# Kernel optimization log

Measured on AMD Instinct MI355X. Metric: run time of the kernel, lower is better.

Reference implementation:

```python
import jax, jax.numpy as jnp
import numpy as np

VOCAB, EMBED, HIDDEN = 29, 64, 256
B, SEQ = 8, 257  # T = SEQ-1 = 256


def setup_inputs() -> dict:
    key = jax.random.key(0)
    ks = jax.random.split(key, 16)
    s = 0.02
    embed = jax.random.normal(ks[0], (VOCAB, EMBED), jnp.float32) * s
    embed = embed.at[0].set(0.0)  # padding_idx = PAD_TOKEN = 0
    d = dict(
        x=jax.random.randint(ks[1], (B, SEQ), 0, VOCAB),
        embed=embed,
        W_ih0=jax.random.normal(ks[2], (HIDDEN, EMBED), jnp.float32) * s,
        b_ih0=jax.random.normal(ks[3], (HIDDEN,), jnp.float32) * s,
        W_hh0=jax.random.normal(ks[4], (HIDDEN, HIDDEN), jnp.float32) * s,
        b_hh0=jax.random.normal(ks[5], (HIDDEN,), jnp.float32) * s,
        W_ih1=jax.random.normal(ks[6], (HIDDEN, HIDDEN), jnp.float32) * s,
        b_ih1=jax.random.normal(ks[7], (HIDDEN,), jnp.float32) * s,
        W_hh1=jax.random.normal(ks[8], (HIDDEN, HIDDEN), jnp.float32) * s,
        b_hh1=jax.random.normal(ks[9], (HIDDEN,), jnp.float32) * s,
        Wq=jax.random.normal(ks[10], (HIDDEN, HIDDEN), jnp.float32) * s,
        Wk=jax.random.normal(ks[11], (HIDDEN, HIDDEN), jnp.float32) * s,
        v=jax.random.normal(ks[12], (HIDDEN,), jnp.float32) * s,
        Wfc=jax.random.normal(ks[13], (VOCAB, 2 * HIDDEN), jnp.float32) * s,
        bfc=jax.random.normal(ks[14], (VOCAB,), jnp.float32) * s,
    )
    return d


def _forward(x, embed, W_ih0, b_ih0, W_hh0, b_hh0, W_ih1, b_ih1, W_hh1, b_hh1,
             Wq, Wk, v, Wfc, bfc):
    inp = x[:, :-1]                       # (B, T)
    emb = embed[inp]                      # (B, T, E); dropout = identity (eval)
    Bb, T, _ = emb.shape
    H = W_hh0.shape[0]

    # 2-layer Elman RNN via scan over time
    def step(carry, e_t):
        h0, h1 = carry
        h0 = jnp.tanh(e_t @ W_ih0.T + b_ih0 + h0 @ W_hh0.T + b_hh0)
        h1 = jnp.tanh(h0 @ W_ih1.T + b_ih1 + h1 @ W_hh1.T + b_hh1)
        return (h0, h1), h1

    init = (jnp.zeros((Bb, H), emb.dtype), jnp.zeros((Bb, H), emb.dtype))
    _, hs = jax.lax.scan(step, init, jnp.swapaxes(emb, 0, 1))  # (T, B, H)
    Hs = jnp.swapaxes(hs, 0, 1)           # (B, T, H) = all_hidden

    # Bahdanau additive self-attention over strictly-past hidden states
    q = Hs @ Wq.T                         # (B, T, H)
    k = Hs @ Wk.T                         # (B, T, H)
    e = jnp.tanh(q[:, :, None, :] + k[:, None, :, :])   # (B, T, T, H)
    scores = jnp.einsum('btsh,h->bts', e, v)             # (B, T, T)
    causal = jnp.tril(jnp.ones((T, T), bool), k=-1)      # s < t strictly
    scores = jnp.where(causal[None], scores, jnp.float32(-1e9))
    alpha = jax.nn.softmax(scores, axis=-1)
    ctx = jnp.einsum('bts,bsh->bth', alpha, Hs)          # (B, T, H)
    ctx = ctx * (jnp.arange(T) > 0)[None, :, None]       # t=0: zero context

    out = jnp.concatenate([Hs, ctx], axis=-1) @ Wfc.T + bfc  # (B, T, V)
    return out


def reference(x, embed, W_ih0, b_ih0, W_hh0, b_hh0, W_ih1, b_ih1, W_hh1, b_hh1,
              Wq, Wk, v, Wfc, bfc):
    return _forward(x, embed, W_ih0, b_ih0, W_hh0, b_hh0, W_ih1, b_ih1,
                    W_hh1, b_hh1, Wq, Wk, v, Wfc, bfc)
```

## Files before the change

### kernel.cpp

```cpp
#include <hip/hip_runtime.h>

#define HID   256
#define BATCH 8
#define TT    256
#define SEQL  257
#define VOCAB 29
#define EMB   64
#define TG    4
#define CH    8
#define NCHK  (TT / CH)

typedef _Float16 f16;
typedef f16  f16x8 __attribute__((ext_vector_type(8)));
typedef float f32x4 __attribute__((ext_vector_type(4)));

__device__ __forceinline__ float fast_tanh(float x) {
    float e = exp2f(x * 2.8853900817779268f);
    return 1.0f - 2.0f * __builtin_amdgcn_rcpf(1.0f + e);
}

__global__ __launch_bounds__(512) void mega_kernel(
    const int* __restrict__ x, const float* __restrict__ embed,
    const float* __restrict__ Wih0, const float* __restrict__ bih0,
    const float* __restrict__ bhh0, const float* __restrict__ Whh0,
    const float* __restrict__ Wih1, const float* __restrict__ Whh1,
    const float* __restrict__ bih1, const float* __restrict__ bhh1,
    const float* __restrict__ Wq, const float* __restrict__ Wk,
    float* __restrict__ C0, float* __restrict__ Q,
    float* __restrict__ Hs, float* __restrict__ tkT, int* __restrict__ flags)
{
    __shared__ f16 hbuf[2][HID];
    __shared__ __align__(16) f16 stg[CH][HID];
    __shared__ float er[CH][EMB];
    int tid = threadIdx.x;
    int wave = tid >> 6, lane = tid & 63;
    int lrow = lane & 15, lkg = lane >> 4;
    int role = blockIdx.x >> 3;
    int b = blockIdx.x & 7;
    int i0 = wave * 32 + lrow, i1 = i0 + 16;
    const f32x4 Z = {0.f, 0.f, 0.f, 0.f};

#define WAITF(idx, val)                                                             \
    {                                                                               \
        if (tid == 0) {                                                             \
            while (__hip_atomic_load(&flags[idx], __ATOMIC_ACQUIRE,                 \
                                     __HIP_MEMORY_SCOPE_AGENT) < (val))             \
                __builtin_amdgcn_s_sleep(2);                                        \
        }                                                                           \
        __syncthreads();                                                            \
    }
#define POSTF(idx, val)                                                             \
    {                                                                               \
        __syncthreads();                                                            \
        if (tid == 0) {                                                             \
            __threadfence();                                                        \
            __hip_atomic_store(&flags[idx], (val), __ATOMIC_RELEASE,                \
                               __HIP_MEMORY_SCOPE_AGENT);                           \
        }                                                                           \
    }

    f16x8 a[8];
#pragma unroll
    for (int kt = 0; kt < 8; ++kt)
#pragma unroll
        for (int e = 0; e < 8; ++e) a[kt][e] = (f16)0.f;

    if (role == 0) {
        int i = tid & 255, half = tid >> 8;
        float base = bih0[i] + bhh0[i];
        const float* wr = Wih0 + i * EMB;
        for (int ch = 0; ch < NCHK; ++ch) {
            int tb = ch * CH;
            { int tt = tid >> 6, j = tid & 63;
              er[tt][j] = embed[x[b * SEQL + tb + tt] * EMB + j]; }
            __syncthreads();
            float a0 = base, a1 = base, a2 = base, a3 = base;
            for (int j = 0; j < EMB; j += 4) {
                float4 w = *(const float4*)&wr[j];
                float4 h0 = *(const float4*)&er[half * 4 + 0][j];
                float4 h1 = *(const float4*)&er[half * 4 + 1][j];
                float4 h2 = *(const float4*)&er[half * 4 + 2][j];
                float4 h3 = *(const float4*)&er[half * 4 + 3][j];
                a0 += h0.x * w.x + h0.y * w.y + h0.z * w.z + h0.w * w.w;
                a1 += h1.x * w.x + h1.y * w.y + h1.z * w.z + h1.w * w.w;
                a2 += h2.x * w.x + h2.y * w.y + h2.z * w.z + h2.w * w.w;
                a3 += h3.x * w.x + h3.y * w.y + h3.z * w.z + h3.w * w.w;
            }
            C0[((size_t)(tb + half * 4 + 0) * BATCH + b) * HID + i] = a0;
            C0[((size_t)(tb + half * 4 + 1) * BATCH + b) * HID + i] = a1;
            C0[((size_t)(tb + half * 4 + 2) * BATCH + b) * HID + i] = a2;
            C0[((size_t)(tb + half * 4 + 3) * BATCH + b) * HID + i] = a3;
            POSTF(b, ch + 1)
        }
    } else if (role == 1) {
        for (int idx = tid; idx < 2 * HID; idx += 512) ((f16*)hbuf)[idx] = (f16)0.f;
        f16x8 bf[8][2];
#pragma unroll
        for (int kt = 0; kt < 8; ++kt)
#pragma unroll
            for (int ct = 0; ct < 2; ++ct) {
                int n = wave * 32 + ct * 16 + lrow;
                const float* src = Whh0 + n * HID + kt * 32 + lkg * 8;
                f16x8 v;
#pragma unroll
                for (int e = 0; e < 8; ++e) v[e] = (f16)src[e];
                bf[kt][ct] = v;
            }
        __syncthreads();
        const float* cp = C0 + b * HID;
        float c0 = 0.f, c1 = 0.f;
        f16* hp = (f16*)(Q + (size_t)b * TT * HID);

#define ASTEP(CUR, NXT)                                                             \
    {                                                                               \
        float cn0 = cp[i0];                                                         \
        float cn1 = cp[i1];                                                         \
        cp += BATCH * HID;                                                          \
        if (lrow == 0) {                                                            \
            _Pragma("unroll")                                                       \
            for (int kt = 0; kt < 8; ++kt)                                          \
                a[kt] = *(const f16x8*)&hbuf[CUR][kt * 32 + lkg * 8];               \
        }                                                                           \
        f32x4 p00 = __builtin_amdgcn_mfma_f32_16x16x32_f16(a[0], bf[0][0], Z, 0, 0, 0); \
        f32x4 p01 = __builtin_amdgcn_mfma_f32_16x16x32_f16(a[0], bf[0][1], Z, 0, 0, 0); \
        f32x4 p10 = __builtin_amdgcn_mfma_f32_16x16x32_f16(a[2], bf[2][0], Z, 0, 0, 0); \
        f32x4 p11 = __builtin_amdgcn_mfma_f32_16x16x32_f16(a[2], bf[2][1], Z, 0, 0, 0); \
        f32x4 p20 = __builtin_amdgcn_mfma_f32_16x16x32_f16(a[4], bf[4][0], Z, 0, 0, 0); \
        f32x4 p21 = __builtin_amdgcn_mfma_f32_16x16x32_f16(a[4], bf[4][1], Z, 0, 0, 0); \
        f32x4 p30 = __builtin_amdgcn_mfma_f32_16x16x32_f16(a[6], bf[6][0], Z, 0, 0, 0); \
        f32x4 p31 = __builtin_amdgcn_mfma_f32_16x16x32_f16(a[6], bf[6][1], Z, 0, 0, 0); \
        p00 = __builtin_amdgcn_mfma_f32_16x16x32_f16(a[1], bf[1][0], p00, 0, 0, 0); \
        p01 = __builtin_amdgcn_mfma_f32_16x16x32_f16(a[1], bf[1][1], p01, 0, 0, 0); \
        p10 = __builtin_amdgcn_mfma_f32_16x16x32_f16(a[3], bf[3][0], p10, 0, 0, 0); \
        p11 = __builtin_amdgcn_mfma_f32_16x16x32_f16(a[3], bf[3][1], p11, 0, 0, 0); \
        p20 = __builtin_amdgcn_mfma_f32_16x16x32_f16(a[5], bf[5][0], p20, 0, 0, 0); \
        p21 = __builtin_amdgcn_mfma_f32_16x16x32_f16(a[5], bf[5][1], p21, 0, 0, 0); \
        p30 = __builtin_amdgcn_mfma_f32_16x16x32_f16(a[7], bf[7][0], p30, 0, 0, 0); \
        p31 = __builtin_amdgcn_mfma_f32_16x16x32_f16(a[7], bf[7][1], p31, 0, 0, 0); \
        float v0 = fast_tanh(((p00[0] + p10[0]) + (p20[0] + p30[0])) + c0);         \
        float v1 = fast_tanh(((p01[0] + p11[0]) + (p21[0] + p31[0])) + c1);         \
        f16 hv0 = (f16)v0, hv1 = (f16)v1;                                           \
        if (lane < 16) {                                                            \
            hbuf[NXT][i0] = hv0;                                                    \
            hbuf[NXT][i1] = hv1;                                                    \
            hp[i0] = hv0;                                                           \
            hp[i1] = hv1;                                                           \
        }                                                                           \
        hp += 2 * HID;                                                              \
        c0 = cn0; c1 = cn1;                                                         \
        asm volatile("s_waitcnt lgkmcnt(0)\n\ts_barrier" ::: "memory");             \
    }

        for (int ch = 0; ch < NCHK; ++ch) {
            WAITF(b, (ch + 2 < NCHK) ? ch + 2 : NCHK)
            if (ch == 0) { c0 = cp[i0]; c1 = cp[i1]; cp += BATCH * HID; }
            ASTEP(0, 1) ASTEP(1, 0) ASTEP(0, 1) ASTEP(1, 0)
            ASTEP(0, 1) ASTEP(1, 0) ASTEP(0, 1) ASTEP(1, 0)
            POSTF(8 + b, ch + 1)
        }
#undef ASTEP
    } else if (role == 2) {
        f16x8 bfI[8][2];
#pragma unroll
        for (int kt = 0; kt < 8; ++kt)
#pragma unroll
            for (int ct = 0; ct < 2; ++ct) {
                int n = wave * 32 + ct * 16 + lrow;
                const float* src = Wih1 + n * HID + kt * 32 + lkg * 8;
                f16x8 v;
#pragma unroll
                for (int e = 0; e < 8; ++e) v[e] = (f16)src[e];
                bfI[kt][ct] = v;
            }
        int col0 = wave * 32 + (lane & 15), col1 = col0 + 16;
        float bv0 = bih1[col0] + bhh1[col0];
        float bv1 = bih1[col1] + bhh1[col1];
        float* qb = Q + (size_t)b * TT * HID;

        for (int ch = 0; ch < NCHK; ++ch) {
            WAITF(8 + b, ch + 1)
            if (tid < 256) {
                int tp = tid >> 5, seg = tid & 31;
                *(f16x8*)&stg[tp][seg * 8] =
                    *(const f16x8*)((const f16*)(qb + (size_t)(ch * CH + tp) * HID) + seg * 8);
            }
            __syncthreads();
            if (lrow < 8) {
#pragma unroll
                for (int kt = 0; kt < 8; ++kt)
                    a[kt] = *(const f16x8*)&stg[lrow][kt * 32 + lkg * 8];
            }
            f32x4 u0 = __builtin_amdgcn_mfma_f32_16x16x32_f16(a[0], bfI[0][0], Z, 0, 0, 0);
            f32x4 u1 = __builtin_amdgcn_mfma_f32_16x16x32_f16(a[0], bfI[0][1], Z, 0, 0, 0);
#pragma unroll
            for (int kt = 1; kt < 8; ++kt) {
                u0 = __builtin_amdgcn_mfma_f32_16x16x32_f16(a[kt], bfI[kt][0], u0, 0, 0, 0);
                u1 = __builtin_amdgcn_mfma_f32_16x16x32_f16(a[kt], bfI[kt][1], u1, 0, 0, 0);
            }
            if (lane < 32) {
                float* co = qb + (size_t)(ch * CH + (lane >> 4) * 4) * HID;
                co[0 * HID + col0] = u0[0] + bv0;
                co[1 * HID + col0] = u0[1] + bv0;
                co[2 * HID + col0] = u0[2] + bv0;
                co[3 * HID + col0] = u0[3] + bv0;
                co[0 * HID + col1] = u1[0] + bv1;
                co[1 * HID + col1] = u1[1] + bv1;
                co[2 * HID + col1] = u1[2] + bv1;
                co[3 * HID + col1] = u1[3] + bv1;
            }
            POSTF(16 + b, ch + 1)
        }
    } else if (role == 3) {
        for (int idx = tid; idx < 2 * HID; idx += 512) ((f16*)hbuf)[idx] = (f16)0.f;
        f16x8 bf[8][2];
#pragma unroll
        for (int kt = 0; kt < 8; ++kt)
#pragma unroll
            for (int ct = 0; ct < 2; ++ct) {
                int n = wave * 32 + ct * 16 + lrow;
                const float* src = Whh1 + n * HID + kt * 32 + lkg * 8;
                f16x8 v;
#pragma unroll
                for (int e = 0; e < 8; ++e) v[e] = (f16)src[e];
                bf[kt][ct] = v;
            }
        __syncthreads();
        float* ho = Hs + (size_t)b * TT * HID;
        const float* cq = Q + (size_t)b * TT * HID;

#define CSTEP(CUR, NXT, CV0, CV1)                                                   \
    {                                                                               \
        if (lrow == 0) {                                                            \
            _Pragma("unroll")                                                       \
            for (int kt = 0; kt < 8; ++kt)                                          \
                a[kt] = *(const f16x8*)&hbuf[CUR][kt * 32 + lkg * 8];               \
        }                                                                           \
        f32x4 p00 = __builtin_amdgcn_mfma_f32_16x16x32_f16(a[0], bf[0][0], Z, 0, 0, 0); \
        f32x4 p01 = __builtin_amdgcn_mfma_f32_16x16x32_f16(a[0], bf[0][1], Z, 0, 0, 0); \
        f32x4 p10 = __builtin_amdgcn_mfma_f32_16x16x32_f16(a[2], bf[2][0], Z, 0, 0, 0); \
        f32x4 p11 = __builtin_amdgcn_mfma_f32_16x16x32_f16(a[2], bf[2][1], Z, 0, 0, 0); \
        f32x4 p20 = __builtin_amdgcn_mfma_f32_16x16x32_f16(a[4], bf[4][0], Z, 0, 0, 0); \
        f32x4 p21 = __builtin_amdgcn_mfma_f32_16x16x32_f16(a[4], bf[4][1], Z, 0, 0, 0); \
        f32x4 p30 = __builtin_amdgcn_mfma_f32_16x16x32_f16(a[6], bf[6][0], Z, 0, 0, 0); \
        f32x4 p31 = __builtin_amdgcn_mfma_f32_16x16x32_f16(a[6], bf[6][1], Z, 0, 0, 0); \
        p00 = __builtin_amdgcn_mfma_f32_16x16x32_f16(a[1], bf[1][0], p00, 0, 0, 0); \
        p01 = __builtin_amdgcn_mfma_f32_16x16x32_f16(a[1], bf[1][1], p01, 0, 0, 0); \
        p10 = __builtin_amdgcn_mfma_f32_16x16x32_f16(a[3], bf[3][0], p10, 0, 0, 0); \
        p11 = __builtin_amdgcn_mfma_f32_16x16x32_f16(a[3], bf[3][1], p11, 0, 0, 0); \
        p20 = __builtin_amdgcn_mfma_f32_16x16x32_f16(a[5], bf[5][0], p20, 0, 0, 0); \
        p21 = __builtin_amdgcn_mfma_f32_16x16x32_f16(a[5], bf[5][1], p21, 0, 0, 0); \
        p30 = __builtin_amdgcn_mfma_f32_16x16x32_f16(a[7], bf[7][0], p30, 0, 0, 0); \
        p31 = __builtin_amdgcn_mfma_f32_16x16x32_f16(a[7], bf[7][1], p31, 0, 0, 0); \
        float v0 = fast_tanh(((p00[0] + p10[0]) + (p20[0] + p30[0])) + CV0);        \
        float v1 = fast_tanh(((p01[0] + p11[0]) + (p21[0] + p31[0])) + CV1);        \
        if (lane < 16) {                                                            \
            hbuf[NXT][i0] = (f16)v0;                                                \
            hbuf[NXT][i1] = (f16)v1;                                                \
            ho[i0] = v0;                                                            \
            ho[i1] = v1;                                                            \
        }                                                                           \
        ho += HID;                                                                  \
        asm volatile("s_waitcnt lgkmcnt(0)\n\ts_barrier" ::: "memory");             \
    }

        for (int ch = 0; ch < NCHK; ++ch) {
            WAITF(16 + b, ch + 1)
            const float* cc = cq + (size_t)ch * CH * HID;
            float d00 = cc[0*HID+i0], d01 = cc[0*HID+i1];
            float d10 = cc[1*HID+i0], d11 = cc[1*HID+i1];
            float d20 = cc[2*HID+i0], d21 = cc[2*HID+i1];
            float d30 = cc[3*HID+i0], d31 = cc[3*HID+i1];
            float d40 = cc[4*HID+i0], d41 = cc[4*HID+i1];
            float d50 = cc[5*HID+i0], d51 = cc[5*HID+i1];
            float d60 = cc[6*HID+i0], d61 = cc[6*HID+i1];
            float d70 = cc[7*HID+i0], d71 = cc[7*HID+i1];
            CSTEP(0, 1, d00, d01) CSTEP(1, 0, d10, d11)
            CSTEP(0, 1, d20, d21) CSTEP(1, 0, d30, d31)
            CSTEP(0, 1, d40, d41) CSTEP(1, 0, d50, d51)
            CSTEP(0, 1, d60, d61) CSTEP(1, 0, d70, d71)
            POSTF(24 + b, ch + 1)
        }
#undef CSTEP
    } else {
        const float* W = (role == 4) ? Wq : Wk;
        f16x8 bfW[8][2];
#pragma unroll
        for (int kt = 0; kt < 8; ++kt)
#pragma unroll
            for (int ct = 0; ct < 2; ++ct) {
                int n = wave * 32 + ct * 16 + lrow;
                const float* src = W + n * HID + kt * 32 + lkg * 8;
                f16x8 v;
#pragma unroll
                for (int e = 0; e < 8; ++e) v[e] = (f16)src[e];
                bfW[kt][ct] = v;
            }
        int col0 = wave * 32 + (lane & 15), col1 = col0 + 16;
        const float* hsb = Hs + (size_t)b * TT * HID;
        float* qb = Q + (size_t)b * TT * HID;

        for (int ch = 0; ch < NCHK; ++ch) {
            WAITF(24 + b, ch + 1)
            if (tid < 256) {
                const float* src = hsb + (size_t)ch * CH * HID + tid * 8;
                float4 v0 = *(const float4*)&src[0];
                float4 v1 = *(const float4*)&src[4];
                f16x8 h = { (f16)v0.x, (f16)v0.y, (f16)v0.z, (f16)v0.w,
                            (f16)v1.x, (f16)v1.y, (f16)v1.z, (f16)v1.w };
                *(f16x8*)((f16*)stg + tid * 8) = h;
            }
            __syncthreads();
            if (lrow < 8) {
#pragma unroll
                for (int kt = 0; kt < 8; ++kt)
                    a[kt] = *(const f16x8*)&stg[lrow][kt * 32 + lkg * 8];
            }
            f32x4 u0 = __builtin_amdgcn_mfma_f32_16x16x32_f16(a[0], bfW[0][0], Z, 0, 0, 0);
            f32x4 u1 = __builtin_amdgcn_mfma_f32_16x16x32_f16(a[0], bfW[0][1], Z, 0, 0, 0);
#pragma unroll
            for (int kt = 1; kt < 8; ++kt) {
                u0 = __builtin_amdgcn_mfma_f32_16x16x32_f16(a[kt], bfW[kt][0], u0, 0, 0, 0);
                u1 = __builtin_amdgcn_mfma_f32_16x16x32_f16(a[kt], bfW[kt][1], u1, 0, 0, 0);
            }
            if (lane < 32) {
                int tb2 = ch * CH + (lane >> 4) * 4;
                if (role == 4) {
                    float* co = qb + (size_t)tb2 * HID;
                    co[0 * HID + col0] = fast_tanh(u0[0]);
                    co[1 * HID + col0] = fast_tanh(u0[1]);
                    co[2 * HID + col0] = fast_tanh(u0[2]);
                    co[3 * HID + col0] = fast_tanh(u0[3]);
                    co[0 * HID + col1] = fast_tanh(u1[0]);
                    co[1 * HID + col1] = fast_tanh(u1[1]);
                    co[2 * HID + col1] = fast_tanh(u1[2]);
                    co[3 * HID + col1] = fast_tanh(u1[3]);
                } else {
                    float4 s0 = { fast_tanh(u0[0]), fast_tanh(u0[1]),
                                  fast_tanh(u0[2]), fast_tanh(u0[3]) };
                    float4 s1 = { fast_tanh(u1[0]), fast_tanh(u1[1]),
                                  fast_tanh(u1[2]), fast_tanh(u1[3]) };
                    *(float4*)&tkT[((size_t)b * HID + col0) * TT + tb2] = s0;
                    *(float4*)&tkT[((size_t)b * HID + col1) * TT + tb2] = s1;
                }
            }
            __syncthreads();
        }
    }
#undef WAITF
#undef POSTF
}

__global__ __launch_bounds__(256) void attn_kernel(
    const float* __restrict__ tq, const float* __restrict__ tkT,
    const float* __restrict__ vvec, const float* __restrict__ Hs,
    const float* __restrict__ Wfc, const float* __restrict__ bfc,
    float* __restrict__ out)
{
    int b  = blockIdx.x & 7;
    int t0 = (blockIdx.x >> 3) * TG;
    int tid = threadIdx.x;
    int wave = tid >> 6, lane = tid & 63;
    __shared__ float qs[TG][HID], vs[HID], alpha[TG][HID];
    __shared__ float cvec[TG][8][68];
    __shared__ float redm[4][TG], reds[4][TG];
#pragma unroll
    for (int j = 0; j < TG; ++j)
        qs[j][tid] = tq[((size_t)b * TT + t0 + j) * HID + tid];
    vs[tid] = vvec[tid];
    __syncthreads();

    float sc[TG];
#pragma unroll
    for (int j = 0; j < TG; ++j) sc[j] = -1e30f;
    if ((wave << 6) < t0 + TG) {
        const float* kT = tkT + (size_t)b * HID * TT + tid;
        float a0 = 0.f, a1 = 0.f, a2 = 0.f, a3 = 0.f;
        for (int jj = 0; jj < HID; jj += 4) {
            float k0 = kT[(size_t)(jj + 0) * TT];
            float k1 = kT[(size_t)(jj + 1) * TT];
            float k2 = kT[(size_t)(jj + 2) * TT];
            float k3 = kT[(size_t)(jj + 3) * TT];
            float4 vv = *(const float4*)&vs[jj];
            float4 q0 = *(const float4*)&qs[0][jj];
            float4 q1 = *(const float4*)&qs[1][jj];
            float4 q2 = *(const float4*)&qs[2][jj];
            float4 q3 = *(const float4*)&qs[3][jj];
#define TADD(qc, kc, vc, acc) { float num = qc + kc; float den = __builtin_fmaf(qc, kc, 1.f); acc += vc * num * __builtin_amdgcn_rcpf(den); }
            TADD(q0.x, k0, vv.x, a0) TADD(q0.y, k1, vv.y, a0) TADD(q0.z, k2, vv.z, a0) TADD(q0.w, k3, vv.w, a0)
            TADD(q1.x, k0, vv.x, a1) TADD(q1.y, k1, vv.y, a1) TADD(q1.z, k2, vv.z, a1) TADD(q1.w, k3, vv.w, a1)
            TADD(q2.x, k0, vv.x, a2) TADD(q2.y, k1, vv.y, a2) TADD(q2.z, k2, vv.z, a2) TADD(q2.w, k3, vv.w, a2)
            TADD(q3.x, k0, vv.x, a3) TADD(q3.y, k1, vv.y, a3) TADD(q3.z, k2, vv.z, a3) TADD(q3.w, k3, vv.w, a3)
#undef TADD
        }
        if (tid < t0 + 0) sc[0] = a0;
        if (tid < t0 + 1) sc[1] = a1;
        if (tid < t0 + 2) sc[2] = a2;
        if (tid < t0 + 3) sc[3] = a3;
    }
    float m0 = sc[0], m1 = sc[1], m2 = sc[2], m3 = sc[3];
#pragma unroll
    for (int off = 32; off; off >>= 1) {
        m0 = fmaxf(m0, __shfl_down(m0, off));
        m1 = fmaxf(m1, __shfl_down(m1, off));
        m2 = fmaxf(m2, __shfl_down(m2, off));
        m3 = fmaxf(m3, __shfl_down(m3, off));
    }
    if (lane == 0) { redm[wave][0] = m0; redm[wave][1] = m1; redm[wave][2] = m2; redm[wave][3] = m3; }
    __syncthreads();
    float ej[TG];
#pragma unroll
    for (int j = 0; j < TG; ++j) {
        float m = fmaxf(fmaxf(redm[0][j], redm[1][j]), fmaxf(redm[2][j], redm[3][j]));
        ej[j] = (tid < t0 + j) ? exp2f((sc[j] - m) * 1.4426950408889634f) : 0.f;
    }
    float z0 = ej[0], z1 = ej[1], z2 = ej[2], z3 = ej[3];
#pragma unroll
    for (int off = 32; off; off >>= 1) {
        z0 += __shfl_down(z0, off);
        z1 += __shfl_down(z1, off);
        z2 += __shfl_down(z2, off);
        z3 += __shfl_down(z3, off);
    }
    if (lane == 0) { reds[wave][0] = z0; reds[wave][1] = z1; reds[wave][2] = z2; reds[wave][3] = z3; }
    __syncthreads();
#pragma unroll
    for (int j = 0; j < TG; ++j) {
        float z = reds[0][j] + reds[1][j] + reds[2][j] + reds[3][j];
        alpha[j][tid] = (t0 + j == 0) ? 0.f : ej[j] * __builtin_amdgcn_rcpf(z);
    }
    __syncthreads();

    float c0 = 0.f, c1 = 0.f, c2 = 0.f, c3 = 0.f;
    const float* hb = Hs + (size_t)b * TT * HID;
    for (int s = 0; s < t0 + TG; s += 4) {
        float4 av0 = *(const float4*)&alpha[0][s];
        float4 av1 = *(const float4*)&alpha[1][s];
        float4 av2 = *(const float4*)&alpha[2][s];
        float4 av3 = *(const float4*)&alpha[3][s];
        float h0 = hb[(s + 0) * HID + tid];
        float h1 = hb[(s + 1) * HID + tid];
        float h2 = hb[(s + 2) * HID + tid];
        float h3 = hb[(s + 3) * HID + tid];
        c0 += av0.x * h0 + av0.y * h1 + av0.z * h2 + av0.w * h3;
        c1 += av1.x * h0 + av1.y * h1 + av1.z * h2 + av1.w * h3;
        c2 += av2.x * h0 + av2.y * h1 + av2.z * h2 + av2.w * h3;
        c3 += av3.x * h0 + av3.y * h1 + av3.z * h2 + av3.w * h3;
    }
    {
        int ph = tid >> 6, jj = tid & 63;
        cvec[0][ph][jj] = hb[(size_t)(t0 + 0) * HID + tid]; cvec[0][4 + ph][jj] = c0;
        cvec[1][ph][jj] = hb[(size_t)(t0 + 1) * HID + tid]; cvec[1][4 + ph][jj] = c1;
        cvec[2][ph][jj] = hb[(size_t)(t0 + 2) * HID + tid]; cvec[2][4 + ph][jj] = c2;
        cvec[3][ph][jj] = hb[(size_t)(t0 + 3) * HID + tid]; cvec[3][4 + ph][jj] = c3;
    }
    __syncthreads();

    if (tid < VOCAB * 8) {
        int o = tid >> 3, p = tid & 7;
        const float* wr = Wfc + o * 2 * HID + p * 64;
#pragma unroll
        for (int j = 0; j < TG; ++j) {
            const float* cv = &cvec[j][p][0];
            float a = 0.f;
            for (int jj = 0; jj < 64; jj += 4) {
                float4 w  = *(const float4*)&wr[jj];
                float4 cc = *(const float4*)&cv[jj];
                a += w.x * cc.x + w.y * cc.y + w.z * cc.z + w.w * cc.w;
            }
            a += __shfl_down(a, 4);
            a += __shfl_down(a, 2);
            a += __shfl_down(a, 1);
            if (p == 0) out[((size_t)b * TT + t0 + j) * VOCAB + o] = a + bfc[o];
        }
    }
}

extern "C" void kernel_launch(void* const* d_in, const int* in_sizes, int n_in,
                              void* d_out, int out_size, void* d_ws, size_t ws_size,
                              hipStream_t stream)
{
    (void)in_sizes; (void)n_in; (void)out_size; (void)ws_size;
    const int*   x     = (const int*)d_in[0];
    const float* embed = (const float*)d_in[1];
    const float* Wih0  = (const float*)d_in[2];
    const float* bih0  = (const float*)d_in[3];
    const float* Whh0  = (const float*)d_in[4];
    const float* bhh0  = (const float*)d_in[5];
    const float* Wih1  = (const float*)d_in[6];
    const float* bih1  = (const float*)d_in[7];
    const float* Whh1  = (const float*)d_in[8];
    const float* bhh1  = (const float*)d_in[9];
    const float* Wq    = (const float*)d_in[10];
    const float* Wk    = (const float*)d_in[11];
    const float* vvec  = (const float*)d_in[12];
    const float* Wfc   = (const float*)d_in[13];
    const float* bfc   = (const float*)d_in[14];
    float* out = (float*)d_out;
    float* ws  = (float*)d_ws;

    const size_t SZ = (size_t)TT * BATCH * HID;
    float* C0  = ws;
    float* Hs  = ws + SZ;
    float* Q   = ws + 2 * SZ;
    float* tkT = ws + 3 * SZ;
    int* flags = (int*)d_out;

    hipMemsetAsync(flags, 0, 32 * sizeof(int), stream);
    mega_kernel<<<48, 512, 0, stream>>>(x, embed, Wih0, bih0, bhh0, Whh0,
                                        Wih1, Whh1, bih1, bhh1, Wq, Wk,
                                        C0, Q, Hs, tkT, flags);
    attn_kernel<<<512, 256, 0, stream>>>(Q, tkT, vvec, Hs, Wfc, bfc, out);
}
```

Baseline: 243.1 us.

## Move layer-0 input projection into separate parallel pre-kernel, drop role and flag waits

The embedding lookup and input projection for layer 0 now run in their own fully parallel kernel of 256 blocks, instead of as a pipelined producer role inside the persistent kernel. The layer-0 recurrence no longer waits on producer flags, the flag count and role count shrink (48 to 40 blocks), and the separate memset is replaced by the pre-kernel zeroing the flags. The cost is an extra kernel launch and a serial dependency before the recurrence can start, traded for removing spin-wait synchronisation from the critical recurrent chain.

Result: faster. 231.6 us (-4.7%).

```diff
diff --git a/kernel.cpp b/kernel.cpp
--- a/kernel.cpp
+++ b/kernel.cpp
@@ -19,19 +19,50 @@
     return 1.0f - 2.0f * __builtin_amdgcn_rcpf(1.0f + e);
 }
 
-__global__ __launch_bounds__(512) void mega_kernel(
+__global__ __launch_bounds__(256) void pre0_kernel(
     const int* __restrict__ x, const float* __restrict__ embed,
     const float* __restrict__ Wih0, const float* __restrict__ bih0,
-    const float* __restrict__ bhh0, const float* __restrict__ Whh0,
-    const float* __restrict__ Wih1, const float* __restrict__ Whh1,
-    const float* __restrict__ bih1, const float* __restrict__ bhh1,
-    const float* __restrict__ Wq, const float* __restrict__ Wk,
-    float* __restrict__ C0, float* __restrict__ Q,
-    float* __restrict__ Hs, float* __restrict__ tkT, int* __restrict__ flags)
+    const float* __restrict__ bhh0, float* __restrict__ C0, int* __restrict__ flags)
+{
+    if (blockIdx.x == 0 && threadIdx.x < 32) flags[threadIdx.x] = 0;
+    int b  = blockIdx.x & 7;
+    int t0 = (blockIdx.x >> 3) * 8;
+    int tid = threadIdx.x;
+    __shared__ float er[8][EMB];
+    for (int idx = tid; idx < 8 * EMB; idx += 256) {
+        int tt = idx >> 6, j = idx & 63;
+        er[tt][j] = embed[x[b * SEQL + t0 + tt] * EMB + j];
+    }
+    __syncthreads();
+    int i = tid;
+    float base = bih0[i] + bhh0[i];
+    float acc[8];
+#pragma unroll
+    for (int tt = 0; tt < 8; ++tt) acc[tt] = base;
+    const float* wr = Wih0 + i * EMB;
+    for (int j = 0; j < EMB; j += 4) {
+        float4 w = *(const float4*)&wr[j];
+#pragma unroll
+        for (int tt = 0; tt < 8; ++tt) {
+            float4 h = *(const float4*)&er[tt][j];
+            acc[tt] += h.x * w.x + h.y * w.y + h.z * w.z + h.w * w.w;
+        }
+    }
+#pragma unroll
+    for (int tt = 0; tt < 8; ++tt)
+        C0[((t0 + tt) * BATCH + b) * HID + i] = acc[tt];
+}
+
+__global__ __launch_bounds__(512) void mega_kernel(
+    const float* __restrict__ Whh0, const float* __restrict__ Wih1,
+    const float* __restrict__ Whh1, const float* __restrict__ bih1,
+    const float* __restrict__ bhh1, const float* __restrict__ Wq,
+    const float* __restrict__ Wk, const float* __restrict__ C0,
+    float* __restrict__ Q, float* __restrict__ Hs,
+    float* __restrict__ tkT, int* __restrict__ flags)
 {
     __shared__ f16 hbuf[2][HID];
     __shared__ __align__(16) f16 stg[CH][HID];
-    __shared__ float er[CH][EMB];
     int tid = threadIdx.x;
     int wave = tid >> 6, lane = tid & 63;
     int lrow = lane & 15, lkg = lane >> 4;
@@ -66,33 +97,6 @@
         for (int e = 0; e < 8; ++e) a[kt][e] = (f16)0.f;
 
     if (role == 0) {
-        int i = tid & 255, half = tid >> 8;
-        float base = bih0[i] + bhh0[i];
-        const float* wr = Wih0 + i * EMB;
-        for (int ch = 0; ch < NCHK; ++ch) {
-            int tb = ch * CH;
-            { int tt = tid >> 6, j = tid & 63;
-              er[tt][j] = embed[x[b * SEQL + tb + tt] * EMB + j]; }
-            __syncthreads();
-            float a0 = base, a1 = base, a2 = base, a3 = base;
-            for (int j = 0; j < EMB; j += 4) {
-                float4 w = *(const float4*)&wr[j];
-                float4 h0 = *(const float4*)&er[half * 4 + 0][j];
-                float4 h1 = *(const float4*)&er[half * 4 + 1][j];
-                float4 h2 = *(const float4*)&er[half * 4 + 2][j];
-                float4 h3 = *(const float4*)&er[half * 4 + 3][j];
-                a0 += h0.x * w.x + h0.y * w.y + h0.z * w.z + h0.w * w.w;
-                a1 += h1.x * w.x + h1.y * w.y + h1.z * w.z + h1.w * w.w;
-                a2 += h2.x * w.x + h2.y * w.y + h2.z * w.z + h2.w * w.w;
-                a3 += h3.x * w.x + h3.y * w.y + h3.z * w.z + h3.w * w.w;
-            }
-            C0[((size_t)(tb + half * 4 + 0) * BATCH + b) * HID + i] = a0;
-            C0[((size_t)(tb + half * 4 + 1) * BATCH + b) * HID + i] = a1;
-            C0[((size_t)(tb + half * 4 + 2) * BATCH + b) * HID + i] = a2;
-            C0[((size_t)(tb + half * 4 + 3) * BATCH + b) * HID + i] = a3;
-            POSTF(b, ch + 1)
-        }
-    } else if (role == 1) {
         for (int idx = tid; idx < 2 * HID; idx += 512) ((f16*)hbuf)[idx] = (f16)0.f;
         f16x8 bf[8][2];
 #pragma unroll
@@ -108,7 +112,8 @@
             }
         __syncthreads();
         const float* cp = C0 + b * HID;
-        float c0 = 0.f, c1 = 0.f;
+        float c0 = cp[i0], c1 = cp[i1];
+        cp += BATCH * HID;
         f16* hp = (f16*)(Q + (size_t)b * TT * HID);
 
 #define ASTEP(CUR, NXT)                                                             \
@@ -146,20 +151,18 @@
             hp[i0] = hv0;                                                           \
             hp[i1] = hv1;                                                           \
         }                                                                           \
-        hp += 2 * HID;                                                              \
+        hp += 2 * HID;    \
         c0 = cn0; c1 = cn1;                                                         \
         asm volatile("s_waitcnt lgkmcnt(0)\n\ts_barrier" ::: "memory");             \
     }
 
         for (int ch = 0; ch < NCHK; ++ch) {
-            WAITF(b, (ch + 2 < NCHK) ? ch + 2 : NCHK)
-            if (ch == 0) { c0 = cp[i0]; c1 = cp[i1]; cp += BATCH * HID; }
             ASTEP(0, 1) ASTEP(1, 0) ASTEP(0, 1) ASTEP(1, 0)
             ASTEP(0, 1) ASTEP(1, 0) ASTEP(0, 1) ASTEP(1, 0)
-            POSTF(8 + b, ch + 1)
+            POSTF(b, ch + 1)
         }
 #undef ASTEP
-    } else if (role == 2) {
+    } else if (role == 1) {
         f16x8 bfI[8][2];
 #pragma unroll
         for (int kt = 0; kt < 8; ++kt)
@@ -178,7 +181,7 @@
         float* qb = Q + (size_t)b * TT * HID;
 
         for (int ch = 0; ch < NCHK; ++ch) {
-            WAITF(8 + b, ch + 1)
+            WAITF(b, ch + 1)
             if (tid < 256) {
                 int tp = tid >> 5, seg = tid & 31;
                 *(f16x8*)&stg[tp][seg * 8] =
@@ -208,9 +211,9 @@
                 co[2 * HID + col1] = u1[2] + bv1;
                 co[3 * HID + col1] = u1[3] + bv1;
             }
-            POSTF(16 + b, ch + 1)
-        }
-    } else if (role == 3) {
+            POSTF(8 + b, ch + 1)
+        }
+    } else if (role == 2) {
         for (int idx = tid; idx < 2 * HID; idx += 512) ((f16*)hbuf)[idx] = (f16)0.f;
         f16x8 bf[8][2];
 #pragma unroll
@@ -264,7 +267,7 @@
     }
 
         for (int ch = 0; ch < NCHK; ++ch) {
-            WAITF(16 + b, ch + 1)
+            WAITF(8 + b, ch + 1)
             const float* cc = cq + (size_t)ch * CH * HID;
             float d00 = cc[0*HID+i0], d01 = cc[0*HID+i1];
             float d10 = cc[1*HID+i0], d11 = cc[1*HID+i1];
@@ -278,11 +281,11 @@
             CSTEP(0, 1, d20, d21) CSTEP(1, 0, d30, d31)
             CSTEP(0, 1, d40, d41) CSTEP(1, 0, d50, d51)
             CSTEP(0, 1, d60, d61) CSTEP(1, 0, d70, d71)
-            POSTF(24 + b, ch + 1)
+            POSTF(16 + b, ch + 1)
         }
 #undef CSTEP
     } else {
-        const float* W = (role == 4) ? Wq : Wk;
+        const float* W = (role == 3) ? Wq : Wk;
         f16x8 bfW[8][2];
 #pragma unroll
         for (int kt = 0; kt < 8; ++kt)
@@ -300,7 +303,7 @@
         float* qb = Q + (size_t)b * TT * HID;
 
         for (int ch = 0; ch < NCHK; ++ch) {
-            WAITF(24 + b, ch + 1)
+            WAITF(16 + b, ch + 1)
             if (tid < 256) {
                 const float* src = hsb + (size_t)ch * CH * HID + tid * 8;
                 float4 v0 = *(const float4*)&src[0];
@@ -324,7 +327,7 @@
             }
             if (lane < 32) {
                 int tb2 = ch * CH + (lane >> 4) * 4;
-                if (role == 4) {
+                if (role == 3) {
                     float* co = qb + (size_t)tb2 * HID;
                     co[0 * HID + col0] = fast_tanh(u0[0]);
                     co[1 * HID + col0] = fast_tanh(u0[1]);
@@ -505,9 +508,8 @@
     float* tkT = ws + 3 * SZ;
     int* flags = (int*)d_out;
 
-    hipMemsetAsync(flags, 0, 32 * sizeof(int), stream);
-    mega_kernel<<<48, 512, 0, stream>>>(x, embed, Wih0, bih0, bhh0, Whh0,
-                                        Wih1, Whh1, bih1, bhh1, Wq, Wk,
+    pre0_kernel<<<256, 256, 0, stream>>>(x, embed, Wih0, bih0, bhh0, C0, flags);
+    mega_kernel<<<40, 512, 0, stream>>>(Whh0, Wih1, Whh1, bih1, bhh1, Wq, Wk,
                                         C0, Q, Hs, tkT, flags);
     attn_kernel<<<512, 256, 0, stream>>>(Q, tkT, vvec, Hs, Wfc, bfc, out);
 }
```
